# Optimization experiments

Measured on AMD Instinct MI355X. Metric: run time of the kernel, lower is better.

Reference implementation:

```python
import jax, jax.numpy as jnp
import numpy as np

B, S, H = 8, 4096, 512

def setup_inputs() -> dict:
    key = jax.random.key(0)
    k1, k2 = jax.random.split(key)
    lstm_out = jax.random.normal(k1, (B, S, H), dtype=jnp.float32)
    W = jax.random.normal(k2, (2 * H, H), dtype=jnp.float32) * (1.0 / np.sqrt(H))
    b = jnp.zeros((2 * H,), dtype=jnp.float32)
    return {"lstm_out": lstm_out, "W": W, "b": b}

def reference(lstm_out, W, b):
    # noise_net: Linear(H, 2H) + Softplus
    noise = jax.nn.softplus(jnp.einsum('bsh,oh->bso', lstm_out, W) + b)  # [B,S,2H]
    Q = noise[:, :, :H]   # process noise
    R = noise[:, :, H:]   # observation noise

    def step(carry, inp):
        state, P = carry
        z, q, r = inp                      # each [B,H]
        P_pred = P + q
        K = P_pred / (P_pred + r + 1e-6)
        state = state + K * (z - state)
        P = (1.0 - K) * P_pred
        return (state, P), state

    state0 = lstm_out[:, 0, :]
    P0 = jnp.full_like(state0, 0.1)
    # time-major for scan: [S,B,H]
    xs = (jnp.swapaxes(lstm_out, 0, 1),
          jnp.swapaxes(Q, 0, 1),
          jnp.swapaxes(R, 0, 1))
    _, states = jax.lax.scan(step, (state0, P0), xs)  # [S,B,H]
    return jnp.swapaxes(states, 0, 1)  # [B,S,H]
```

## Files before the change

kernel.cpp:

```cpp
#include <hip/hip_runtime.h>
#include <hip/hip_bf16.h>

#define B_ 8
#define S_ 4096
#define H_ 512

using short8 = __attribute__((ext_vector_type(8))) short;
using f32x4  = __attribute__((ext_vector_type(4))) float;

__device__ __forceinline__ float bf2f(unsigned u16) {
    return __uint_as_float(u16 << 16);
}
__device__ __forceinline__ unsigned pk2bf(float x, float y) {
    __hip_bfloat162 h = __float22bfloat162_rn(make_float2(x, y));
    return *reinterpret_cast<unsigned*>(&h);
}
__device__ __forceinline__ float softplus_f(float x) {
    float sp = __logf(1.0f + __expf(x));
    return x > 15.0f ? x : sp;
}

typedef __attribute__((address_space(1))) void* gbl_ptr_t;
typedef __attribute__((address_space(3))) void* lds_ptr_t;
__device__ __forceinline__ void gload_lds16(const void* g, void* l) {
    __builtin_amdgcn_global_load_lds((gbl_ptr_t)g, (lds_ptr_t)l, 16, 0, 0);
}

#define BAR() do { asm volatile("" ::: "memory"); \
                   __builtin_amdgcn_s_barrier(); \
                   asm volatile("" ::: "memory"); } while (0)

#define ASZ4 4194304u
#define TOT4 4325376u

__global__ __launch_bounds__(256)
void convert_bf16(const float* __restrict__ A, const float* __restrict__ Wm,
                  uint2* __restrict__ dst) {
    for (unsigned i = blockIdx.x * 256u + threadIdx.x; i < TOT4; i += 2048u * 256u) {
        const float4* p = (i < ASZ4) ? ((const float4*)A) + i
                                     : ((const float4*)Wm) + (i - ASZ4);
        const float4 v = *p;
        uint2 o;
        o.x = pk2bf(v.x, v.y);
        o.y = pk2bf(v.z, v.w);
        dst[i] = o;
    }
}

#define TM 256
#define TN 256
#define KT 64

__global__ __launch_bounds__(512, 2)
void gemm_softplus(const unsigned short* __restrict__ Ab,
                   const unsigned short* __restrict__ Wb,
                   const float* __restrict__ bias,
                   unsigned* __restrict__ QR) {
    extern __shared__ __align__(16) unsigned short smem[];
    unsigned short* Asm = smem;
    unsigned short* Bsm = smem + 32768;

    const int bid     = blockIdx.x;
    const int logical = (bid & 7) * 64 + (bid >> 3);
    const int bm = logical >> 2;
    const int bn = logical & 3;

    const int t      = threadIdx.x;
    const int wave   = t >> 6;
    const int lane   = t & 63;
    const int wave_m = wave >> 2;
    const int wave_n = wave & 3;
    const int wm  = wave_m * 128;
    const int wn  = wave_n * 64;
    const int l15 = lane & 15;
    const int l4  = lane >> 4;

    const int m0 = bm * TM;

    const int q_  = lane >> 2;
    const int g_  = lane & 3;
    const int sgo = (g_ ^ ((q_ >> 1) & 3)) * 8;
    const int row0 = wave * 16 + q_;
    const int nr0 = bn * 128 + ((row0 >> 6) << 5) + (row0 & 31) + (((row0 >> 5) & 1) << 9);
    const unsigned short* agA0 = Ab + (size_t)(m0 + row0) * 512 + sgo;
    const unsigned short* agA1 = agA0 + (size_t)128 * 512;
    const unsigned short* bgB0 = Wb + (size_t)nr0 * 512 + sgo;
    const unsigned short* bgB1 = bgB0 + (size_t)64 * 512;
    const int sdw = wave * 512;

    const int gsw  = (l4 ^ ((l15 >> 1) & 3)) * 8;
    const int aoff = (wm + l15) * 32 + gsw;
    const int boff = (wn + l15) * 32 + gsw;

    f32x4 acc[8][4] = {};

#define STAGE(tt, kh) do { \
    const int _kc = (tt) * KT + (kh) * 32; \
    const int _db = ((tt) & 1) * 16384 + (kh) * 8192; \
    gload_lds16(agA0 + _kc, Asm + _db + sdw); \
    gload_lds16(agA1 + _kc, Asm + _db + sdw + 4096); \
    gload_lds16(bgB0 + _kc, Bsm + _db + sdw); \
    gload_lds16(bgB1 + _kc, Bsm + _db + sdw + 4096); \
} while (0)

#define MMA16(ibase) do { \
    __builtin_amdgcn_s_setprio(1); \
    _Pragma("unroll") for (int ii = 0; ii < 4; ++ii) \
    _Pragma("unroll") for (int jj = 0; jj < 4; ++jj) \
        acc[(ibase) + ii][jj] = __builtin_amdgcn_mfma_f32_16x16x32_bf16( \
            af[ii], bf[jj], acc[(ibase) + ii][jj], 0, 0, 0); \
    __builtin_amdgcn_s_setprio(0); \
} while (0)

#define TILE(tt, VM0, VM2, DOSTG) do { \
    const unsigned short* _a = Asm + ((tt) & 1) * 16384; \
    const unsigned short* _b = Bsm + ((tt) & 1) * 16384; \
    short8 af[4], bf[4]; \
    BAR();                                \
    if (DOSTG) STAGE((tt) + 1, 0); \
    asm volatile("s_waitcnt vmcnt(" #VM0 ")" ::: "memory"); \
    BAR();                                \
    _Pragma("unroll") for (int jj = 0; jj < 4; ++jj) \
        bf[jj] = *(const short8*)(_b + boff + jj * 512); \
    _Pragma("unroll") for (int ii = 0; ii < 4; ++ii) \
        af[ii] = *(const short8*)(_a + aoff + ii * 512); \
    MMA16(0); \
    _Pragma("unroll") for (int ii = 0; ii < 4; ++ii) \
        af[ii] = *(const short8*)(_a + aoff + (ii + 4) * 512); \
    MMA16(4); \
    if (DOSTG) STAGE((tt) + 1, 1); \
    asm volatile("s_waitcnt vmcnt(" #VM2 ")" ::: "memory"); \
    BAR();                                \
    _Pragma("unroll") for (int jj = 0; jj < 4; ++jj) \
        bf[jj] = *(const short8*)(_b + 8192 + boff + jj * 512); \
    _Pragma("unroll") for (int ii = 0; ii < 4; ++ii) \
        af[ii] = *(const short8*)(_a + 8192 + aoff + ii * 512); \
    MMA16(0); \
    _Pragma("unroll") for (int ii = 0; ii < 4; ++ii) \
        af[ii] = *(const short8*)(_a + 8192 + aoff + (ii + 4) * 512); \
    MMA16(4); \
} while (0)

    STAGE(0, 0); STAGE(0, 1);

    for (int tt = 0; tt < 7; ++tt) TILE(tt, 8, 8, 1);
    TILE(7, 4, 0, 0);

#undef TILE
#undef MMA16
#undef STAGE

#pragma unroll
    for (int j = 0; j < 2; ++j) {
        const int h  = bn * 128 + (wn >> 1) + j * 16 + l15;
        const float bq = bias[h];
        const float br = bias[h + 512];
#pragma unroll
        for (int i = 0; i < 8; ++i) {
            const int mb = m0 + wm + i * 16 + l4 * 4;
#pragma unroll
            for (int r = 0; r < 4; ++r) {
                const float qv = softplus_f(acc[i][j][r] + bq);
                const float rv = softplus_f(acc[i][j + 2][r] + br);
                QR[(size_t)(mb + r) * 512 + h] = pk2bf(qv, rv);
            }
        }
    }
}

#define CHUNK 128
#define WARM 64

__global__ __launch_bounds__(256, 2)
void kalman_scan(const float* __restrict__ z,
                 const unsigned* __restrict__ QR,
                 float* __restrict__ out) {
    const int t     = threadIdx.x;
    const int hb    = blockIdx.x & 1;
    const int b     = (blockIdx.x >> 1) & 7;
    const int chunk = blockIdx.x >> 4;
    const int h     = hb * 256 + t;
    const int s0    = chunk << 7;
    const int sw    = (chunk == 0) ? 0 : (s0 - WARM);
    const size_t base = ((size_t)(b * S_ + sw)) * 512 + h;

    const float*    zp  = z + base;
    const unsigned* qrp = (const unsigned*)QR + base;
    float*          op  = out + base;

    const int ng    = ((s0 + CHUNK) - sw) >> 3;
    const int skipg = (s0 - sw) >> 3;

    float    Z0[8], Z1[8], Z2[8], Z3[8], Z4[8], Z5[8], Z6[8], Z7[8];
    unsigned Q0[8], Q1[8], Q2[8], Q3[8], Q4[8], Q5[8], Q6[8], Q7[8];

#define LOADG(g, Zb, Qb) { const int _o = (g) * 8;                          \
    _Pragma("unroll") for (int u = 0; u < 8; ++u) {                         \
        Zb[u] = zp[(size_t)(_o + u) * 512]; Qb[u] = qrp[(size_t)(_o + u) * 512]; } }

#define COMP(g, Zb, Qb) { const int _o = (g) * 8; const bool _st = (g) >= skipg; \
    _Pragma("unroll") for (int u = 0; u < 8; ++u) {                         \
        const float q  = bf2f(Qb[u] & 0xffffu);                             \
        const float r  = bf2f(Qb[u] >> 16);                                 \
        const float Pp = P + q, rr = r + 1e-6f;                             \
        const float K  = Pp * __builtin_amdgcn_rcpf(Pp + rr);               \
        state = fmaf(K, Zb[u] - state, state); P = rr * K;                  \
        if (_st) op[(size_t)(_o + u) * 512] = state; } }

    LOADG(0, Z0, Q0); LOADG(1, Z1, Q1); LOADG(2, Z2, Q2); LOADG(3, Z3, Q3);

    float state = Z0[0];
    float P = 0.1f;

    for (int g = 0; g < ng; g += 8) {
        if (g + 4  < ng) LOADG(g + 4,  Z4, Q4); COMP(g,     Z0, Q0);
        if (g + 5  < ng) LOADG(g + 5,  Z5, Q5); COMP(g + 1, Z1, Q1);
        if (g + 6  < ng) LOADG(g + 6,  Z6, Q6); COMP(g + 2, Z2, Q2);
        if (g + 7  < ng) LOADG(g + 7,  Z7, Q7); COMP(g + 3, Z3, Q3);
        if (g + 8  < ng) LOADG(g + 8,  Z0, Q0); COMP(g + 4, Z4, Q4);
        if (g + 9  < ng) LOADG(g + 9,  Z1, Q1); COMP(g + 5, Z5, Q5);
        if (g + 10 < ng) LOADG(g + 10, Z2, Q2); COMP(g + 6, Z6, Q6);
        if (g + 11 < ng) LOADG(g + 11, Z3, Q3); COMP(g + 7, Z7, Q7);
    }
#undef LOADG
#undef COMP
}

extern "C" void kernel_launch(void* const* d_in, const int* in_sizes, int n_in,
                              void* d_out, int out_size, void* d_ws, size_t ws_size,
                              hipStream_t stream) {
    const float* lstm = (const float*)d_in[0];
    const float* Wm   = (const float*)d_in[1];
    const float* bias = (const float*)d_in[2];

    unsigned* QRw = (unsigned*)d_ws;

    unsigned short* Abf = (unsigned short*)d_out;
    unsigned short* Wbf = (unsigned short*)((char*)d_out + (32u << 20));

    static bool lds_set = false;
    if (!lds_set) {
        hipFuncSetAttribute(reinterpret_cast<const void*>(&gemm_softplus),
                            hipFuncAttributeMaxDynamicSharedMemorySize, 131072);
        lds_set = true;
    }

    hipLaunchKernelGGL(convert_bf16, dim3(2048), dim3(256), 0, stream,
                       lstm, Wm, (uint2*)Abf);

    hipLaunchKernelGGL(gemm_softplus, dim3(512), dim3(512), 131072, stream,
                       Abf, Wbf, bias, QRw);

    hipLaunchKernelGGL(kalman_scan, dim3(512), dim3(256), 0, stream,
                       lstm, QRw, (float*)d_out);
}
```

Before: 197.8 us.

## Use 4-slot K=32 LDS ring in GEMM and larger scan chunks

The GEMM main loop moves from double-buffered K=64 tiles, which needed two barriers per half-tile, to a four-slot ring of K=32 slices with three slices of prefetch in flight and graded vmcnt waits. The aim is deeper global-to-LDS prefetch and fewer stalls between MFMA bursts. Separately, the Kalman scan chunk grows from 128 to 256 timesteps and the grid halves. This cuts the share of redundant warm-up steps but leaves fewer blocks to hide memory latency.

```diff
diff --git a/kernel.cpp b/kernel.cpp
--- a/kernel.cpp
+++ b/kernel.cpp
@@ -49,7 +49,7 @@
 
 #define TM 256
 #define TN 256
-#define KT 64
+#define KS 32
 
 __global__ __launch_bounds__(512, 2)
 void gemm_softplus(const unsigned short* __restrict__ Ab,
@@ -94,13 +94,13 @@
 
     f32x4 acc[8][4] = {};
 
-#define STAGE(tt, kh) do { \
-    const int _kc = (tt) * KT + (kh) * 32; \
-    const int _db = ((tt) & 1) * 16384 + (kh) * 8192; \
-    gload_lds16(agA0 + _kc, Asm + _db + sdw); \
-    gload_lds16(agA1 + _kc, Asm + _db + sdw + 4096); \
-    gload_lds16(bgB0 + _kc, Bsm + _db + sdw); \
-    gload_lds16(bgB1 + _kc, Bsm + _db + sdw + 4096); \
+#define STAGE(s) do { \
+    const int _kc = (s) * KS; \
+    const int _sl = ((s) & 3) * 8192; \
+    gload_lds16(agA0 + _kc, Asm + _sl + sdw); \
+    gload_lds16(agA1 + _kc, Asm + _sl + sdw + 4096); \
+    gload_lds16(bgB0 + _kc, Bsm + _sl + sdw); \
+    gload_lds16(bgB1 + _kc, Bsm + _sl + sdw + 4096); \
 } while (0)
 
 #define MMA16(ibase) do { \
@@ -112,14 +112,13 @@
     __builtin_amdgcn_s_setprio(0); \
 } while (0)
 
-#define TILE(tt, VM0, VM2, DOSTG) do { \
-    const unsigned short* _a = Asm + ((tt) & 1) * 16384; \
-    const unsigned short* _b = Bsm + ((tt) & 1) * 16384; \
+#define SLICE(g, VMN, DOSTG) do { \
+    const unsigned short* _a = Asm + ((g) & 3) * 8192; \
+    const unsigned short* _b = Bsm + ((g) & 3) * 8192; \
+    if (DOSTG) STAGE((g) + 3); \
+    asm volatile("s_waitcnt vmcnt(" #VMN ")" ::: "memory"); \
+    BAR(); \
     short8 af[4], bf[4]; \
-    BAR();                                \
-    if (DOSTG) STAGE((tt) + 1, 0); \
-    asm volatile("s_waitcnt vmcnt(" #VM0 ")" ::: "memory"); \
-    BAR();                                \
     _Pragma("unroll") for (int jj = 0; jj < 4; ++jj) \
         bf[jj] = *(const short8*)(_b + boff + jj * 512); \
     _Pragma("unroll") for (int ii = 0; ii < 4; ++ii) \
@@ -128,25 +127,17 @@
     _Pragma("unroll") for (int ii = 0; ii < 4; ++ii) \
         af[ii] = *(const short8*)(_a + aoff + (ii + 4) * 512); \
     MMA16(4); \
-    if (DOSTG) STAGE((tt) + 1, 1); \
-    asm volatile("s_waitcnt vmcnt(" #VM2 ")" ::: "memory"); \
-    BAR();                                \
-    _Pragma("unroll") for (int jj = 0; jj < 4; ++jj) \
-        bf[jj] = *(const short8*)(_b + 8192 + boff + jj * 512); \
-    _Pragma("unroll") for (int ii = 0; ii < 4; ++ii) \
-        af[ii] = *(const short8*)(_a + 8192 + aoff + ii * 512); \
-    MMA16(0); \
-    _Pragma("unroll") for (int ii = 0; ii < 4; ++ii) \
-        af[ii] = *(const short8*)(_a + 8192 + aoff + (ii + 4) * 512); \
-    MMA16(4); \
+    BAR(); \
 } while (0)
 
-    STAGE(0, 0); STAGE(0, 1);
-
-    for (int tt = 0; tt < 7; ++tt) TILE(tt, 8, 8, 1);
-    TILE(7, 4, 0, 0);
-
-#undef TILE
+    STAGE(0); STAGE(1); STAGE(2);
+
+    for (int g = 0; g < 13; ++g) SLICE(g, 12, 1);
+    SLICE(13, 8, 0);
+    SLICE(14, 4, 0);
+    SLICE(15, 0, 0);
+
+#undef SLICE
 #undef MMA16
 #undef STAGE
 
@@ -168,7 +159,7 @@
     }
 }
 
-#define CHUNK 128
+#define CHUNK 256
 #define WARM 64
 
 __global__ __launch_bounds__(256, 2)
@@ -180,7 +171,7 @@
     const int b     = (blockIdx.x >> 1) & 7;
     const int chunk = blockIdx.x >> 4;
     const int h     = hb * 256 + t;
-    const int s0    = chunk << 7;
+    const int s0    = chunk << 8;
     const int sw    = (chunk == 0) ? 0 : (s0 - WARM);
     const size_t base = ((size_t)(b * S_ + sw)) * 512 + h;
 
@@ -251,6 +242,6 @@
     hipLaunchKernelGGL(gemm_softplus, dim3(512), dim3(512), 131072, stream,
                        Abf, Wbf, bias, QRw);
 
-    hipLaunchKernelGGL(kalman_scan, dim3(512), dim3(256), 0, stream,
+    hipLaunchKernelGGL(kalman_scan, dim3(256), dim3(256), 0, stream,
                        lstm, QRw, (float*)d_out);
 }
```

After: 195.8 us. About the same (-1.0%).
